# Optimization experiments

Measured on AMD Instinct MI355X. Metric: run time of the kernel, lower is better.

Reference implementation:

```python
import jax, jax.numpy as jnp
import numpy as np
from math import comb

K = 10  # Bernstein polynomial order (matches Parameter(torch.Tensor(K+1)))


def _norm_adj(adj):
    # A = (adj > 0); Ahat = D^-1/2 A D^-1/2 (sym gcn norm used by get_laplacian)
    A = (adj > 0).astype(adj.dtype)                     # [B, n, n]
    deg = A.sum(-1)                                     # [B, n]
    dis = jnp.where(deg > 0, jax.lax.rsqrt(jnp.maximum(deg, 1e-12)), 0.0)
    return dis[..., :, None] * A * dis[..., None, :]


def _bern_conv(x, Ahat, coe, W, b):
    # BernConv: linear transform then Bernstein-polynomial spectral filter
    # out = sum_{k=0}^{K} relu(coe)[k] * C(K,k)/2^K * L^k (2I-L)^{K-k} h,
    # with L = I - Ahat, so (2I-L) v = v + Ahat v, L v = v - Ahat v.
    h = x @ W + b                                       # [B, n, out]
    T = jax.nn.relu(coe)
    binom = jnp.asarray([comb(K, k) / (2.0 ** K) for k in range(K + 1)],
                        dtype=x.dtype)
    c = binom * T                                       # [K+1]
    mm = lambda v: jnp.einsum('bij,bjh->bih', Ahat, v)
    # powers of (2I - L): tmp[j] = (I + Ahat)^j h
    tmp = [h]
    for _ in range(K):
        t = tmp[-1]
        tmp.append(t + mm(t))
    # Horner accumulation of sum_{i=1..K} c[i] * L^i tmp[K-i]
    Lv = lambda v: v - mm(v)
    acc = c[K] * tmp[0]
    for i in range(K - 1, 0, -1):
        acc = Lv(acc) + c[i] * tmp[K - i]
    return c[0] * tmp[K] + Lv(acc)


def reference(adj, x, coe, W0, b0, W1, b1, W2, b2, Wout, bout):
    # dropout is identity (eval mode / rate 0)
    Ahat = _norm_adj(adj)
    h0 = jax.nn.relu(_bern_conv(x, Ahat, coe, W0, b0))                     # [B,n,hd]
    h1 = jax.nn.relu(_bern_conv(jnp.concatenate([x, h0], -1), Ahat, coe, W1, b1))
    h2 = jax.nn.relu(_bern_conv(jnp.concatenate([x, h0, h1], -1), Ahat, coe, W2, b2))
    bern = jnp.concatenate([h0, h1, h2], -1) + x                            # [B,n,H]
    return bern @ Wout + bout                                               # [B,n,H]


def setup_inputs() -> dict:
    key = jax.random.key(0)
    ks = jax.random.split(key, 12)
    B, n, H = 8, 2048, 768
    hd = H // 3
    p_edge = 0.005  # avg degree ~10, sparse graph
    adj = (jax.random.uniform(ks[0], (B, n, n)) < p_edge).astype(jnp.float32)
    x = jax.random.normal(ks[1], (B, n, H), dtype=jnp.float32)
    s = 0.02
    inp = {
        'adj': adj,
        'x': x,
        'coe': jnp.ones((K + 1,), jnp.float32),
        'W0': jax.random.normal(ks[2], (H, hd), jnp.float32) * s,
        'b0': jnp.zeros((hd,), jnp.float32),
        'W1': jax.random.normal(ks[3], (H + hd, hd), jnp.float32) * s,
        'b1': jnp.zeros((hd,), jnp.float32),
        'W2': jax.random.normal(ks[4], (H + 2 * hd, hd), jnp.float32) * s,
        'b2': jnp.zeros((hd,), jnp.float32),
        'Wout': jax.random.normal(ks[5], (H, H), jnp.float32) * s,
        'bout': jnp.zeros((H,), jnp.float32),
    }
    return inp
```

## Files before the change

### kernel.cpp

```cpp
#include <hip/hip_runtime.h>

#define KORD   10
#define MAXDEG 64
#define NB     2048
#define NROWS  16384
#define HD     256
#define XBW    1536

typedef __attribute__((ext_vector_type(8))) short short8;
typedef __attribute__((ext_vector_type(4))) float f32x4;

__device__ inline unsigned short f2bf(float f) {
  union { float f; unsigned u; } v; v.f = f;
  unsigned r = v.u + 0x7fff + ((v.u >> 16) & 1);
  return (unsigned short)(r >> 16);
}
__device__ inline float bf2f(unsigned short b) {
  union { unsigned u; float f; } v; v.u = ((unsigned)b) << 16;
  return v.f;
}

#define AS1 __attribute__((address_space(1)))
#define AS3 __attribute__((address_space(3)))
__device__ inline void gload16(const void* g, void* l) {
  __builtin_amdgcn_global_load_lds((const AS1 void*)g, (AS3 void*)l, 16, 0, 0);
}

__device__ inline double binom_d(int n, int r) {
  if (r < 0 || r > n) return 0.0;
  double v = 1.0;
  for (int i = 1; i <= r; ++i) v = v * (double)(n - r + i) / (double)i;
  return v;
}

__global__ __launch_bounds__(128) void qz_kernel(const float* __restrict__ coe,
                                                 float* __restrict__ qf,
                                                 int* __restrict__ zstate) {
  __shared__ double part[(KORD + 1) * (KORD + 1)];
  __shared__ double qs[KORD + 1];
  const int t = threadIdx.x;
  if (t < (KORD + 1) * (KORD + 1)) {
    const int k = t / (KORD + 1), m = t % (KORD + 1);
    double tt = (double)coe[k];
    if (tt < 0.0) tt = 0.0;
    const double ck = tt * binom_d(KORD, k) / 1024.0;
    double s = 0.0;
    for (int j = 0; j <= k && j <= m; ++j) {
      const int rem = m - j;
      if (rem <= KORD - k) {
        const double term = binom_d(k, j) * binom_d(KORD - k, rem);
        s += (j & 1) ? -term : term;
      }
    }
    part[t] = ck * s;
  }
  __syncthreads();
  if (t <= KORD) {
    double q = 0.0;
    for (int k = 0; k <= KORD; ++k) q += part[k * (KORD + 1) + t];
    qs[t] = q;
    qf[t] = (float)q;
  }
  __syncthreads();
  if (t == 0) {
    zstate[KORD + 1] = 1;
    int z = 1;
    for (int m = KORD; m >= 0; --m) {
      if (qs[m] != 0.0) z = 0;
      zstate[m] = z;
    }
  }
}

__global__ __launch_bounds__(256) void prep_kernel(
    const float* __restrict__ adj, const float* __restrict__ x,
    const float* __restrict__ W0, const float* __restrict__ W1,
    const float* __restrict__ W2, const float* __restrict__ Wout,
    const int* __restrict__ zstate,
    int* __restrict__ cnt, float* __restrict__ dis,
    unsigned short* __restrict__ colidx,
    unsigned short* __restrict__ XB,
    unsigned short* __restrict__ Wt0, unsigned short* __restrict__ Wt1,
    unsigned short* __restrict__ Wt2, unsigned short* __restrict__ WtO) {
  __shared__ float tile[32][33];
  const int blk = blockIdx.x;
  const int t = threadIdx.x;

  if (blk < 4096) {
    if (zstate[1]) return;
    const int wave = t >> 6;
    const int lane = t & 63;
    const int row  = blk * 4 + wave;
    const float4* arow4 = (const float4*)(adj + (size_t)row * NB);
    unsigned short* ci = colidx + (size_t)row * MAXDEG;
    float4 v[8];
#pragma unroll
    for (int i = 0; i < 8; ++i) v[i] = arow4[i * 64 + lane];
    const unsigned long long lower = (1ull << lane) - 1ull;
    int base = 0;
#pragma unroll
    for (int i = 0; i < 8; ++i) {
      const int col = i * 256 + lane * 4;
      const int b0 = v[i].x > 0.f, b1 = v[i].y > 0.f;
      const int b2 = v[i].z > 0.f, b3 = v[i].w > 0.f;
      const unsigned long long m0 = __ballot(b0), m1 = __ballot(b1);
      const unsigned long long m2 = __ballot(b2), m3 = __ballot(b3);
      int pre = base + __popcll(m0 & lower) + __popcll(m1 & lower) +
                __popcll(m2 & lower) + __popcll(m3 & lower);
      if (b0) { if (pre < MAXDEG) ci[pre] = (unsigned short)col; ++pre; }
      if (b1) { if (pre < MAXDEG) ci[pre] = (unsigned short)(col + 1); ++pre; }
      if (b2) { if (pre < MAXDEG) ci[pre] = (unsigned short)(col + 2); ++pre; }
      if (b3) { if (pre < MAXDEG) ci[pre] = (unsigned short)(col + 3); ++pre; }
      base += __popcll(m0) + __popcll(m1) + __popcll(m2) + __popcll(m3);
    }
    if (lane == 0) {
      cnt[row] = base > MAXDEG ? MAXDEG : base;
      dis[row] = base > 0 ? rsqrtf((float)base) : 0.0f;
    }
    return;
  }

  if (blk < 6144) {
    const int r0 = (blk - 4096) * 8;
    for (int i = t; i < 8 * 192; i += 256) {
      const int r = r0 + (i / 192);
      const int c = (i % 192) * 4;
      float4 v = *(const float4*)&x[(size_t)r * 768 + c];
      union { unsigned short s[4]; uint2 u; } o;
      o.s[0] = f2bf(v.x); o.s[1] = f2bf(v.y);
      o.s[2] = f2bf(v.z); o.s[3] = f2bf(v.w);
      *(uint2*)&XB[(size_t)r * XBW + c] = o.u;
    }
    return;
  }

  const float* W; unsigned short* Wt; int N, ldt, koff, gx, lb;
  int b = blk - 6144;
  if (b < 192)       { W = W0;   Wt = Wt0; N = 256; ldt = 768;  koff = 0;   gx = 24; lb = b; }
  else if (b < 448)  { W = W1;   Wt = Wt1; N = 256; ldt = 1024; koff = 0;   gx = 32; lb = b - 192; }
  else if (b < 768)  { W = W2;   Wt = Wt2; N = 256; ldt = 1280; koff = 0;   gx = 40; lb = b - 448; }
  else if (b < 1344) { W = Wout; Wt = WtO; N = 768; ldt = 1536; koff = 0;   gx = 24; lb = b - 768; }
  else               { W = Wout; Wt = WtO; N = 768; ldt = 1536; koff = 768; gx = 24; lb = b - 1344; }
  const int k0 = (lb % gx) * 32, n0 = (lb / gx) * 32;
  const int tx = t & 31, ty = t >> 5;
#pragma unroll
  for (int i = 0; i < 4; ++i)
    tile[ty + 8 * i][tx] = W[(size_t)(k0 + ty + 8 * i) * N + n0 + tx];
  __syncthreads();
#pragma unroll
  for (int i = 0; i < 4; ++i)
    Wt[(size_t)(n0 + ty + 8 * i) * ldt + koff + k0 + tx] =
        f2bf(tile[tx][ty + 8 * i]);
}

__global__ __launch_bounds__(256) void mfma_gemm_kernel(
    int Kd,
    const unsigned short* __restrict__ A, int lda,
    const unsigned short* __restrict__ Wt, int ldw,
    const float* __restrict__ bias,
    float* __restrict__ outF, unsigned short* __restrict__ outB, int ldo,
    const float* __restrict__ qf, const int* __restrict__ zstate,
    unsigned short* __restrict__ xb_epi, unsigned short* __restrict__ bern_epi,
    int layer) {
  __shared__ __align__(16) unsigned short Asl[4][128 * 32];
  __shared__ __align__(16) unsigned short Bsl[4][128 * 32];
  const int t    = threadIdx.x;
  const int lane = t & 63;
  const int wid  = t >> 6;
  const int wr   = wid >> 1, wc = wid & 1;

  const int gx  = gridDim.x;
  const int nwg = gx * gridDim.y;
  int bid = blockIdx.y * gx + blockIdx.x;
  if ((nwg & 7) == 0) bid = (bid & 7) * (nwg >> 3) + (bid >> 3);
  const int row0 = (bid / gx) * 128;
  const int col0 = (bid % gx) * 128;

  f32x4 acc[4][4] = {};

  const int swz    = ((lane & 3) ^ ((lane >> 3) & 3)) * 8;
  const int subrow = lane >> 2;
  const int fr = lane & 15;
  const int fq = lane >> 4;

  const int nkt = Kd >> 5;

  auto stage = [&](int kt, int pb) {
    const int kbase = kt << 5;
#pragma unroll
    for (int i = 0; i < 4; ++i) {
      const int c = wid * 4 + i;
      if (c < 8) {
        const int r = row0 + c * 16 + subrow;
        gload16(A + (size_t)r * lda + kbase + swz, &Asl[pb][c * 512]);
      } else {
        const int cc = c - 8;
        const int r = col0 + cc * 16 + subrow;
        gload16(Wt + (size_t)r * ldw + kbase + swz, &Bsl[pb][cc * 512]);
      }
    }
  };

  stage(0, 0);
  if (nkt > 1) stage(1, 1);

  for (int kt = 0; kt < nkt; ++kt) {
    const int pb = kt & 3;
    if (kt + 2 < nkt) {
      stage(kt + 2, (kt + 2) & 3);
      asm volatile("s_waitcnt vmcnt(8)" ::: "memory");
    } else if (kt + 1 < nkt) {
      asm volatile("s_waitcnt vmcnt(4)" ::: "memory");
    } else {
      asm volatile("s_waitcnt vmcnt(0)" ::: "memory");
    }
    __builtin_amdgcn_s_barrier();
    asm volatile("" ::: "memory");

    short8 af[4], bfr[4];
#pragma unroll
    for (int m = 0; m < 4; ++m) {
      const int r = wr * 64 + m * 16 + fr;
      const int colb = (fq * 16) ^ (((r >> 1) & 3) << 4);
      af[m] = *(const short8*)((const char*)&Asl[pb][0] + r * 64 + colb);
    }
#pragma unroll
    for (int n = 0; n < 4; ++n) {
      const int r = wc * 64 + n * 16 + fr;
      const int colb = (fq * 16) ^ (((r >> 1) & 3) << 4);
      bfr[n] = *(const short8*)((const char*)&Bsl[pb][0] + r * 64 + colb);
    }
    __builtin_amdgcn_s_setprio(1);
#pragma unroll
    for (int m = 0; m < 4; ++m)
#pragma unroll
      for (int n = 0; n < 4; ++n)
        acc[m][n] = __builtin_amdgcn_mfma_f32_16x16x32_bf16(af[m], bfr[n],
                                                            acc[m][n], 0, 0, 0);
    __builtin_amdgcn_s_setprio(0);
  }

  int fastepi = 0; float q0 = 0.f;
  if (xb_epi) { fastepi = zstate[1]; q0 = qf[0]; }
#pragma unroll
  for (int n = 0; n < 4; ++n) {
    const int col = col0 + wc * 64 + n * 16 + fr;
    const float bv = bias[col];
#pragma unroll
    for (int m = 0; m < 4; ++m) {
      const int rbase = row0 + wr * 64 + m * 16 + fq * 4;
#pragma unroll
      for (int r = 0; r < 4; ++r) {
        const float v = acc[m][n][r] + bv;
        const size_t rr = (size_t)(rbase + r);
        if (fastepi) {
          const float hv = fmaxf(q0 * v, 0.f);
          const unsigned short hb = f2bf(hv);
          xb_epi[rr * XBW + 768 + layer * HD + col] = hb;
          if (bern_epi)
            bern_epi[rr * 768 + layer * HD + col] =
                f2bf(bf2f(hb) + bf2f(xb_epi[rr * XBW + layer * HD + col]));
        } else if (outB) {
          outB[rr * ldo + col] = f2bf(v);
        } else {
          outF[rr * ldo + col] = v;
        }
      }
    }
  }
}

__global__ __launch_bounds__(256, 1) void horner_kernel(
    const unsigned short* __restrict__ h,
    const int* __restrict__ cnt, const float* __restrict__ dis,
    const unsigned short* __restrict__ colidx,
    const float* __restrict__ qf, const int* __restrict__ zstate,
    unsigned short* __restrict__ XB, unsigned short* __restrict__ bern,
    int layer, int fused) {
  __shared__ float accA[NB * 4];
  __shared__ float accB[NB * 4];
  __shared__ float dls[NB];
  __shared__ int   cls[NB];
  const int blk = blockIdx.x;
  const int b   = blk >> 6;
  const int ch0 = (blk & 63) * 4;
  const int t   = threadIdx.x;
  const size_t rowbase = (size_t)b * NB;

  if (zstate[1]) {
    if (fused) return;
    const float q0 = qf[0];
    for (int r = t; r < NB; r += 256) {
      union { unsigned short s[4]; uint2 u; } iv, ov, xv, bv;
      iv.u = *(const uint2*)&h[(rowbase + r) * HD + ch0];
#pragma unroll
      for (int j = 0; j < 4; ++j)
        ov.s[j] = f2bf(fmaxf(q0 * bf2f(iv.s[j]), 0.f));
      *(uint2*)&XB[(rowbase + r) * XBW + 768 + layer * HD + ch0] = ov.u;
      if (bern) {
        xv.u = *(const uint2*)&XB[(rowbase + r) * XBW + layer * HD + ch0];
#pragma unroll
        for (int j = 0; j < 4; ++j)
          bv.s[j] = f2bf(bf2f(ov.s[j]) + bf2f(xv.s[j]));
        *(uint2*)&bern[(rowbase + r) * 768 + layer * HD + ch0] = bv.u;
      }
    }
    return;
  }

  for (int r = t; r < NB; r += 256) {
    dls[r] = dis[rowbase + r];
    cls[r] = cnt[rowbase + r];
  }
  __syncthreads();
  float* cur = accA;
  float* nxt = accB;
  const int ch = t & 3;
  for (int m = KORD; m >= 0; --m) {
    if (m == 0 || !zstate[m]) {
      const float qm = qf[m];
      const int gather = !zstate[m + 1];
      for (int r = t >> 2; r < NB; r += 64) {
        float s = 0.f;
        if (gather) {
          const int deg = cls[r];
          const float di = dls[r];
          const unsigned short* ci = colidx + (rowbase + r) * MAXDEG;
          for (int e = 0; e < deg; ++e) {
            const int nb = ci[e];
            s += di * dls[nb] * cur[nb * 4 + ch];
          }
        }
        if (qm != 0.f) s += qm * bf2f(h[(rowbase + r) * HD + ch0 + ch]);
        if (m == 0) {
          const float hv = fmaxf(s, 0.f);
          XB[(rowbase + r) * XBW + 768 + layer * HD + ch0 + ch] = f2bf(hv);
          if (bern)
            bern[(rowbase + r) * 768 + layer * HD + ch0 + ch] = f2bf(
                hv + bf2f(XB[(rowbase + r) * XBW + layer * HD + ch0 + ch]));
        } else {
          nxt[r * 4 + ch] = s;
        }
      }
    }
    __syncthreads();
    float* tp = cur; cur = nxt; nxt = tp;
  }
}

extern "C" void kernel_launch(void* const* d_in, const int* in_sizes, int n_in,
                              void* d_out, int out_size, void* d_ws, size_t ws_size,
                              hipStream_t stream) {
  const float* adj  = (const float*)d_in[0];
  const float* x    = (const float*)d_in[1];
  const float* coe  = (const float*)d_in[2];
  const float* W0   = (const float*)d_in[3];
  const float* b0   = (const float*)d_in[4];
  const float* W1   = (const float*)d_in[5];
  const float* b1   = (const float*)d_in[6];
  const float* W2   = (const float*)d_in[7];
  const float* b2   = (const float*)d_in[8];
  const float* Wout = (const float*)d_in[9];
  const float* bout = (const float*)d_in[10];
  float* outp = (float*)d_out;

  unsigned short* bufH = (unsigned short*)outp;

  char* ws = (char*)d_ws;
  size_t off = 0;
  float* qf     = (float*)(ws + off); off += 256;
  int*   zstate = (int*)(ws + off);   off += 256;
  int*   cnt    = (int*)(ws + off);   off += 65536;
  float* dis    = (float*)(ws + off); off += 65536;
  unsigned short* colidx = (unsigned short*)(ws + off); off += (size_t)NROWS * MAXDEG * 2;
  unsigned short* XB     = (unsigned short*)(ws + off); off += (size_t)NROWS * XBW * 2;
  unsigned short* Wt0 = (unsigned short*)(ws + off); off += (size_t)256 * 768 * 2;
  unsigned short* Wt1 = (unsigned short*)(ws + off); off += (size_t)256 * 1024 * 2;
  unsigned short* Wt2 = (unsigned short*)(ws + off); off += (size_t)256 * 1280 * 2;
  unsigned short* WtO = (unsigned short*)(ws + off); off += (size_t)768 * 1536 * 2;
  unsigned short* bern = (unsigned short*)(ws + off);
  const size_t need = off + (size_t)NROWS * 768 * 2;
  const int split = ws_size >= need;
  unsigned short* bernp = split ? bern : (unsigned short*)nullptr;

  hipLaunchKernelGGL(qz_kernel, dim3(1), dim3(128), 0, stream, coe, qf, zstate);
  hipLaunchKernelGGL(prep_kernel, dim3(8064), dim3(256), 0, stream,
                     adj, x, W0, W1, W2, Wout, zstate,
                     cnt, dis, colidx, XB, Wt0, Wt1, Wt2, WtO);

  auto layer = [&](int Kd, const unsigned short* Wt, const float* bias, int l) {
    hipLaunchKernelGGL(mfma_gemm_kernel, dim3(2, 128), dim3(256), 0, stream,
                       Kd, XB, XBW, Wt, Kd, bias, (float*)nullptr, bufH, HD,
                       qf, zstate, XB, bernp, l);
    hipLaunchKernelGGL(horner_kernel, dim3(512), dim3(256), 0, stream,
                       bufH, cnt, dis, colidx, qf, zstate, XB, bernp, l, 1);
  };
  layer(768,  Wt0, b0, 0);
  layer(1024, Wt1, b1, 1);
  layer(1280, Wt2, b2, 2);

  if (split)
    hipLaunchKernelGGL(mfma_gemm_kernel, dim3(6, 128), dim3(256), 0, stream,
                       768, bern, 768, WtO, 1536, bout, outp,
                       (unsigned short*)nullptr, 768,
                       qf, zstate, (unsigned short*)nullptr,
                       (unsigned short*)nullptr, 0);
  else
    hipLaunchKernelGGL(mfma_gemm_kernel, dim3(6, 128), dim3(256), 0, stream,
                       1536, XB, XBW, WtO, 1536, bout, outp,
                       (unsigned short*)nullptr, 768,
                       qf, zstate, (unsigned short*)nullptr,
                       (unsigned short*)nullptr, 0);
}
```

Baseline: 178.1 us.

## Batch the x-part of all three layer GEMMs into one wide GEMM

The x-dependent part of the three layer input projections (x @ W0, x @ W1[:768], x @ W2[:768]) is computed once in a single 768-wide GEMM over x. Layer 0's columns go through the normal epilogue, and the other two partial products are stored as bf16 in a scratch buffer placed after bufH in the output. Layers 1 and 2 then only run GEMMs over the concatenated hidden features (K=256 and 512) and add the precomputed partial in the epilogue. This is meant to avoid re-reading x three times and to use fewer, larger GEMM tiles, at the cost of rounding the partial sums to bf16 and an extra read and write of the scratch buffer.

```diff
diff --git a/kernel.cpp b/kernel.cpp
--- a/kernel.cpp
+++ b/kernel.cpp
@@ -34,11 +34,14 @@
 }
 
 __global__ __launch_bounds__(128) void qz_kernel(const float* __restrict__ coe,
+                                                 const float* __restrict__ b0,
                                                  float* __restrict__ qf,
-                                                 int* __restrict__ zstate) {
+                                                 int* __restrict__ zstate,
+                                                 float* __restrict__ biasX) {
   __shared__ double part[(KORD + 1) * (KORD + 1)];
   __shared__ double qs[KORD + 1];
   const int t = threadIdx.x;
+  for (int i = t; i < 768; i += 128) biasX[i] = i < 256 ? b0[i] : 0.0f;
   if (t < (KORD + 1) * (KORD + 1)) {
     const int k = t / (KORD + 1), m = t % (KORD + 1);
     double tt = (double)coe[k];
@@ -80,8 +83,8 @@
     int* __restrict__ cnt, float* __restrict__ dis,
     unsigned short* __restrict__ colidx,
     unsigned short* __restrict__ XB,
-    unsigned short* __restrict__ Wt0, unsigned short* __restrict__ Wt1,
-    unsigned short* __restrict__ Wt2, unsigned short* __restrict__ WtO) {
+    unsigned short* __restrict__ WtX, unsigned short* __restrict__ WtB1,
+    unsigned short* __restrict__ WtB2, unsigned short* __restrict__ WtO) {
   __shared__ float tile[32][33];
   const int blk = blockIdx.x;
   const int t = threadIdx.x;
@@ -134,13 +137,15 @@
     return;
   }
 
-  const float* W; unsigned short* Wt; int N, ldt, koff, gx, lb;
+  const float* W; unsigned short* Wt; int N, ldt, koff, noff, gx, lb;
   int b = blk - 6144;
-  if (b < 192)       { W = W0;   Wt = Wt0; N = 256; ldt = 768;  koff = 0;   gx = 24; lb = b; }
-  else if (b < 448)  { W = W1;   Wt = Wt1; N = 256; ldt = 1024; koff = 0;   gx = 32; lb = b - 192; }
-  else if (b < 768)  { W = W2;   Wt = Wt2; N = 256; ldt = 1280; koff = 0;   gx = 40; lb = b - 448; }
-  else if (b < 1344) { W = Wout; Wt = WtO; N = 768; ldt = 1536; koff = 0;   gx = 24; lb = b - 768; }
-  else               { W = Wout; Wt = WtO; N = 768; ldt = 1536; koff = 768; gx = 24; lb = b - 1344; }
+  if (b < 192)       { W = W0;             Wt = WtX;  N = 256; ldt = 768;  koff = 0;   noff = 0;   gx = 24; lb = b; }
+  else if (b < 384)  { W = W1;             Wt = WtX;  N = 256; ldt = 768;  koff = 0;   noff = 256; gx = 24; lb = b - 192; }
+  else if (b < 576)  { W = W2;             Wt = WtX;  N = 256; ldt = 768;  koff = 0;   noff = 512; gx = 24; lb = b - 384; }
+  else if (b < 640)  { W = W1 + 768 * 256; Wt = WtB1; N = 256; ldt = 256;  koff = 0;   noff = 0;   gx = 8;  lb = b - 576; }
+  else if (b < 768)  { W = W2 + 768 * 256; Wt = WtB2; N = 256; ldt = 512;  koff = 0;   noff = 0;   gx = 16; lb = b - 640; }
+  else if (b < 1344) { W = Wout;           Wt = WtO;  N = 768; ldt = 1536; koff = 0;   noff = 0;   gx = 24; lb = b - 768; }
+  else               { W = Wout;           Wt = WtO;  N = 768; ldt = 1536; koff = 768; noff = 0;   gx = 24; lb = b - 1344; }
   const int k0 = (lb % gx) * 32, n0 = (lb / gx) * 32;
   const int tx = t & 31, ty = t >> 5;
 #pragma unroll
@@ -149,7 +154,7 @@
   __syncthreads();
 #pragma unroll
   for (int i = 0; i < 4; ++i)
-    Wt[(size_t)(n0 + ty + 8 * i) * ldt + koff + k0 + tx] =
+    Wt[(size_t)(noff + n0 + ty + 8 * i) * ldt + koff + k0 + tx] =
         f2bf(tile[tx][ty + 8 * i]);
 }
 
@@ -158,6 +163,8 @@
     const unsigned short* __restrict__ A, int lda,
     const unsigned short* __restrict__ Wt, int ldw,
     const float* __restrict__ bias,
+    const unsigned short* __restrict__ Cin, int ldc,
+    unsigned short* __restrict__ px, int ldpx, int pxsplit,
     float* __restrict__ outF, unsigned short* __restrict__ outB, int ldo,
     const float* __restrict__ qf, const int* __restrict__ zstate,
     unsigned short* __restrict__ xb_epi, unsigned short* __restrict__ bern_epi,
@@ -251,9 +258,12 @@
       const int rbase = row0 + wr * 64 + m * 16 + fq * 4;
 #pragma unroll
       for (int r = 0; r < 4; ++r) {
-        const float v = acc[m][n][r] + bv;
+        float v = acc[m][n][r] + bv;
         const size_t rr = (size_t)(rbase + r);
-        if (fastepi) {
+        if (Cin) v += bf2f(Cin[rr * ldc + col]);
+        if (col >= pxsplit) {
+          px[rr * ldpx + (col - pxsplit)] = f2bf(v);
+        } else if (fastepi) {
           const float hv = fmaxf(q0 * v, 0.f);
           const unsigned short hb = f2bf(hv);
           xb_epi[rr * XBW + 768 + layer * HD + col] = hb;
@@ -365,50 +375,75 @@
   float* outp = (float*)d_out;
 
   unsigned short* bufH = (unsigned short*)outp;
+  unsigned short* PX   = bufH + (size_t)NROWS * HD;
 
   char* ws = (char*)d_ws;
   size_t off = 0;
   float* qf     = (float*)(ws + off); off += 256;
   int*   zstate = (int*)(ws + off);   off += 256;
+  float* biasX  = (float*)(ws + off); off += 768 * 4;
   int*   cnt    = (int*)(ws + off);   off += 65536;
   float* dis    = (float*)(ws + off); off += 65536;
   unsigned short* colidx = (unsigned short*)(ws + off); off += (size_t)NROWS * MAXDEG * 2;
   unsigned short* XB     = (unsigned short*)(ws + off); off += (size_t)NROWS * XBW * 2;
-  unsigned short* Wt0 = (unsigned short*)(ws + off); off += (size_t)256 * 768 * 2;
-  unsigned short* Wt1 = (unsigned short*)(ws + off); off += (size_t)256 * 1024 * 2;
-  unsigned short* Wt2 = (unsigned short*)(ws + off); off += (size_t)256 * 1280 * 2;
-  unsigned short* WtO = (unsigned short*)(ws + off); off += (size_t)768 * 1536 * 2;
+  unsigned short* WtX  = (unsigned short*)(ws + off); off += (size_t)768 * 768 * 2;
+  unsigned short* WtB1 = (unsigned short*)(ws + off); off += (size_t)256 * 256 * 2;
+  unsigned short* WtB2 = (unsigned short*)(ws + off); off += (size_t)256 * 512 * 2;
+  unsigned short* WtO  = (unsigned short*)(ws + off); off += (size_t)768 * 1536 * 2;
   unsigned short* bern = (unsigned short*)(ws + off);
   const size_t need = off + (size_t)NROWS * 768 * 2;
   const int split = ws_size >= need;
   unsigned short* bernp = split ? bern : (unsigned short*)nullptr;
 
-  hipLaunchKernelGGL(qz_kernel, dim3(1), dim3(128), 0, stream, coe, qf, zstate);
+  hipLaunchKernelGGL(qz_kernel, dim3(1), dim3(128), 0, stream,
+                     coe, b0, qf, zstate, biasX);
   hipLaunchKernelGGL(prep_kernel, dim3(8064), dim3(256), 0, stream,
                      adj, x, W0, W1, W2, Wout, zstate,
-                     cnt, dis, colidx, XB, Wt0, Wt1, Wt2, WtO);
-
-  auto layer = [&](int Kd, const unsigned short* Wt, const float* bias, int l) {
-    hipLaunchKernelGGL(mfma_gemm_kernel, dim3(2, 128), dim3(256), 0, stream,
-                       Kd, XB, XBW, Wt, Kd, bias, (float*)nullptr, bufH, HD,
-                       qf, zstate, XB, bernp, l);
-    hipLaunchKernelGGL(horner_kernel, dim3(512), dim3(256), 0, stream,
-                       bufH, cnt, dis, colidx, qf, zstate, XB, bernp, l, 1);
-  };
-  layer(768,  Wt0, b0, 0);
-  layer(1024, Wt1, b1, 1);
-  layer(1280, Wt2, b2, 2);
+                     cnt, dis, colidx, XB, WtX, WtB1, WtB2, WtO);
+
+  const int PXL = 1 << 30;
+
+  hipLaunchKernelGGL(mfma_gemm_kernel, dim3(6, 128), dim3(256), 0, stream,
+                     768, XB, XBW, WtX, 768, biasX,
+                     (const unsigned short*)nullptr, 0,
+                     PX, 512, 256,
+                     (float*)nullptr, bufH, HD,
+                     qf, zstate, XB, bernp, 0);
+  hipLaunchKernelGGL(horner_kernel, dim3(512), dim3(256), 0, stream,
+                     bufH, cnt, dis, colidx, qf, zstate, XB, bernp, 0, 1);
+
+  hipLaunchKernelGGL(mfma_gemm_kernel, dim3(2, 128), dim3(256), 0, stream,
+                     256, XB + 768, XBW, WtB1, 256, b1,
+                     PX, 512,
+                     (unsigned short*)nullptr, 0, PXL,
+                     (float*)nullptr, bufH, HD,
+                     qf, zstate, XB, bernp, 1);
+  hipLaunchKernelGGL(horner_kernel, dim3(512), dim3(256), 0, stream,
+                     bufH, cnt, dis, colidx, qf, zstate, XB, bernp, 1, 1);
+
+  hipLaunchKernelGGL(mfma_gemm_kernel, dim3(2, 128), dim3(256), 0, stream,
+                     512, XB + 768, XBW, WtB2, 512, b2,
+                     PX + 256, 512,
+                     (unsigned short*)nullptr, 0, PXL,
+                     (float*)nullptr, bufH, HD,
+                     qf, zstate, XB, bernp, 2);
+  hipLaunchKernelGGL(horner_kernel, dim3(512), dim3(256), 0, stream,
+                     bufH, cnt, dis, colidx, qf, zstate, XB, bernp, 2, 1);
 
   if (split)
     hipLaunchKernelGGL(mfma_gemm_kernel, dim3(6, 128), dim3(256), 0, stream,
-                       768, bern, 768, WtO, 1536, bout, outp,
-                       (unsigned short*)nullptr, 768,
+                       768, bern, 768, WtO, 1536, bout,
+                       (const unsigned short*)nullptr, 0,
+                       (unsigned short*)nullptr, 0, PXL,
+                       outp, (unsigned short*)nullptr, 768,
                        qf, zstate, (unsigned short*)nullptr,
                        (unsigned short*)nullptr, 0);
   else
     hipLaunchKernelGGL(mfma_gemm_kernel, dim3(6, 128), dim3(256), 0, stream,
-                       1536, XB, XBW, WtO, 1536, bout, outp,
-                       (unsigned short*)nullptr, 768,
+                       1536, XB, XBW, WtO, 1536, bout,
+                       (const unsigned short*)nullptr, 0,
+                       (unsigned short*)nullptr, 0, PXL,
+                       outp, (unsigned short*)nullptr, 768,
                        qf, zstate, (unsigned short*)nullptr,
                        (unsigned short*)nullptr, 0);
 }
```

New measurement: 228.0 us. 28.0% more time.
